# Performance work log

Measured on AMD Instinct MI355X. Metric: run time of the kernel, lower is better.

Reference implementation:

```python
import jax, jax.numpy as jnp
import numpy as np

B, P, C, H, W = 2, 4, 3, 256, 256
BGH, BGW = 2764, 3856
NOISE_MU, NOISE_SIGMA, NOISE_POISSON, BG_RATIO = 5.0, 1.0, 2.0, 0.1


def setup_inputs() -> dict:
    key = jax.random.key(0)
    k_x, k_bg = jax.random.split(key, 2)
    x = jax.random.uniform(k_x, (B, P, C, H, W), dtype=jnp.float32)
    t = jnp.array([0.05, 0.1, 0.15, 0.2], dtype=jnp.float32)          # Time_init (len p)
    ratio = jnp.ones((P,), dtype=jnp.float32)
    life = jnp.array([100.0, 200.0, 300.0], dtype=jnp.float32)         # flo_life (len c)
    intensity_ratio = jnp.array([1.0, 0.8, 0.6], dtype=jnp.float32)    # flo_intensity_ratio
    bg_file = jax.random.uniform(k_bg, (P, BGH, BGW), dtype=jnp.float32)
    return {"x": x, "t": t, "ratio": ratio, "life": life,
            "intensity_ratio": intensity_ratio, "bg_file": bg_file}


def reference(x, t, ratio, life, intensity_ratio, bg_file):
    b, p, c, h, w = x.shape
    key = jax.random.key(42)
    k_life, k_sig, k_norm, k_p1, k_p2, k_bg1, k_bg2, k_bgn, k_idx = jax.random.split(key, 9)

    # Time = relu((t*ratio)*1000), per-p scalar broadcast over (b,c,h,w)
    Time = jnp.maximum((t * ratio) * 1000.0, 0.0)                      # (p,)

    # tao_i: 9-point linspace around each lifetime, concatenated -> (T,) with T = 9*c
    tao = (life[:, None] + jnp.linspace(-40.0, 40.0, 9)).reshape(-1)   # (9c,)

    Life = life[None, None, :, None, None]                             # (1,1,c,1,1)
    Life_rand = Life + (jax.random.uniform(k_life, (b, p, c, h, w)) - 0.5) * 2.0 * 6.0
    sigma = 6.0
    sigma_rand = sigma + (jax.random.uniform(k_sig, (b, p, c, h, w)) - 0.5) * 2.0 * sigma * 0.05

    tao6 = tao[:, None, None, None, None, None]                        # (T,1,1,1,1,1)
    # Gaussian weights over the tao axis (matches torch's 3.14 constant)
    w_i = jnp.exp(-(tao6 - Life_rand) ** 2 / (2.0 * sigma_rand ** 2)) / (
        jnp.sqrt(jnp.float32(2.0 * 3.14)) * sigma_rand)                # (T,b,p,c,h,w)
    w_i = w_i / w_i.sum(axis=0)

    # tao_gt: sum over c, mean over p, permute -> (b,T,h,w), detached
    tao_gt = jax.lax.stop_gradient(jnp.transpose(w_i.sum(axis=3).mean(axis=2), (1, 0, 2, 3)))

    # decay_metrics = sum_T w_i * exp(-Time/tao); exp term only depends on (T,p)
    et = jnp.exp(-Time[None, :] / tao[:, None])                        # (T,p)
    decay = jnp.einsum('tp,tbpchw->bpchw', et, w_i)                    # (b,p,c,h,w)

    x2 = (x * decay * intensity_ratio[None, None, :, None, None]).sum(axis=2)  # (b,p,h,w)

    # noise(): Normal + Poisson(x/max) + Poisson(const) + x (samples detached in torch)
    xm = x2 / (x2.max() + 0.0001)
    n_int = xm * NOISE_MU + NOISE_SIGMA * jax.random.normal(k_norm, x2.shape)
    p_int = jax.random.poisson(k_p1, jnp.maximum(xm, 0.0)).astype(x2.dtype)
    pois = jax.random.poisson(k_p2, jnp.full(x2.shape, NOISE_POISSON)).astype(x2.dtype)
    x3 = n_int + p_int + pois + x2

    # bg(): scaled background file + noise, random 256x256 row offset
    bg1 = jax.random.uniform(k_bg1, (b, p, 1, 1)) * 0.5 + 0.5
    bg2 = jax.random.uniform(k_bg2, (b, p, 1, 1)) * 0.5 + 0.5
    bgn = jax.random.normal(k_bgn, (b, p, BGH, BGW))
    GRR = (bg_file[None] * bg1 + bgn * bg2) * BG_RATIO                 # (b,p,BGH,BGW)
    idx = jax.random.randint(k_idx, (), 0, 9)
    patch = jax.lax.dynamic_slice(GRR, (0, 0, idx, 0), (b, p, 256, 256))
    x4 = jnp.clip(x3 + patch, 0.0, 255.0) / 255.0

    return (x4, tao_gt, t * ratio, ratio)
```

## Files before the change

kernel.cpp:

```cpp
#include <hip/hip_runtime.h>
#include <cstdint>
#include <cstddef>

#define BB 2
#define PP 4
#define CC 3
#define HWSZ 65536
#define BGH 2764
#define BGW 3856
#define NTAO 27
#define X4_SIZE (BB*PP*HWSZ)
#define TAO_OFF X4_SIZE
#define TAO_SIZE (BB*NTAO*HWSZ)
#define OUT2_OFF (TAO_OFF + TAO_SIZE)
#define NPK 24
#define NBLK_A 2048

__host__ __device__ inline uint32_t rotl32(uint32_t x, int r) {
#ifdef __HIP_DEVICE_COMPILE__
  return __builtin_amdgcn_alignbit(x, x, 32 - r);
#else
  return (x << r) | (x >> (32 - r));
#endif
}

__host__ __device__ inline void tf2x32(uint32_t k0, uint32_t k1,
                                       uint32_t x0, uint32_t x1,
                                       uint32_t& o0, uint32_t& o1) {
  uint32_t ks2 = k0 ^ k1 ^ 0x1BD11BDAu;
  x0 += k0; x1 += k1;
#define TF_RND(r) { x0 += x1; x1 = rotl32(x1, r); x1 ^= x0; }
  TF_RND(13) TF_RND(15) TF_RND(26) TF_RND(6)
  x0 += k1;  x1 += ks2 + 1u;
  TF_RND(17) TF_RND(29) TF_RND(16) TF_RND(24)
  x0 += ks2; x1 += k0 + 2u;
  TF_RND(13) TF_RND(15) TF_RND(26) TF_RND(6)
  x0 += k0;  x1 += k1 + 3u;
  TF_RND(17) TF_RND(29) TF_RND(16) TF_RND(24)
  x0 += k1;  x1 += ks2 + 4u;
  TF_RND(13) TF_RND(15) TF_RND(26) TF_RND(6)
  x0 += ks2; x1 += k0 + 5u;
#undef TF_RND
  o0 = x0; o1 = x1;
}

__host__ __device__ inline uint32_t bits32(uint32_t k0, uint32_t k1, uint32_t e) {
  uint32_t o0, o1;
  tf2x32(k0, k1, 0u, e, o0, o1);
  return o0 ^ o1;
}

static void jax_split(uint32_t k0, uint32_t k1, int n, uint32_t (*keys)[2]) {
  for (int i = 0; i < n; ++i)
    tf2x32(k0, k1, 0u, (uint32_t)i, keys[i][0], keys[i][1]);
}

__host__ __device__ inline float u01(uint32_t bits) {
  uint32_t fb = (bits >> 9) | 0x3F800000u;
  return __builtin_bit_cast(float, fb) - 1.0f;
}

__device__ inline float erfinv_f(float x) {
  float w = -__logf(fmaf(-x, x, 1.0f));
  float p;
  if (w < 5.0f) {
    w = w - 2.5f;
    p = 2.81022636e-08f;
    p = fmaf(p, w, 3.43273939e-07f);
    p = fmaf(p, w, -3.5233877e-06f);
    p = fmaf(p, w, -4.39150654e-06f);
    p = fmaf(p, w, 0.00021858087f);
    p = fmaf(p, w, -0.00125372503f);
    p = fmaf(p, w, -0.00417768164f);
    p = fmaf(p, w, 0.246640727f);
    p = fmaf(p, w, 1.50140941f);
  } else {
    w = __builtin_amdgcn_sqrtf(w) - 3.0f;
    p = -0.000200214257f;
    p = fmaf(p, w, 0.000100950558f);
    p = fmaf(p, w, 0.00134934322f);
    p = fmaf(p, w, -0.00367342844f);
    p = fmaf(p, w, 0.00573950773f);
    p = fmaf(p, w, -0.0076224613f);
    p = fmaf(p, w, 0.00943887047f);
    p = fmaf(p, w, 1.00167406f);
    p = fmaf(p, w, 2.83297682f);
  }
  return p * x;
}

__device__ inline float normal_e(uint32_t k0, uint32_t k1, uint32_t e) {
  float f = u01(bits32(k0, k1, e));
  const float LO = -0.99999994f;
  float u = fmaxf(LO, fmaf(f, 2.0f, LO));
  return 1.41421356237f * erfinv_f(u);
}

struct PCParams {
  uint32_t kn0, kn1;
  uint32_t kb0, kb1;
  uint32_t s1[NPK * 2];
  uint32_t s2[NPK * 2];
  float bg1[8], bg2[8];
  int idx;
};

__device__ inline int pk_count2(const uint32_t* __restrict__ sk,
                                uint32_t e, float T) {
  float P = 1.0f;
  int cnt = 0;
#pragma clang loop unroll(disable)
  for (int i = 0; i < NPK; i += 2) {
    if (!__any(P > T)) break;
    float u0 = u01(bits32(sk[2*i],     sk[2*i+1],     e));
    float u1 = u01(bits32(sk[2*i+2],   sk[2*i+3],     e));
    float P0 = P * u0;
    float P1 = P0 * u1;
    cnt += (P0 > T) ? 1 : 0;
    cnt += (P1 > T) ? 1 : 0;
    P = P1;
  }
  return cnt;
}

__device__ inline float decay_pc(uint32_t kl0, uint32_t kl1, uint32_t ks0,
                                 uint32_t ks1, uint32_t e,
                                 const float (*et)[4], int p, float* tg9) {
  float ul = u01(bits32(kl0, kl1, e));
  float us = u01(bits32(ks0, ks1, e));
  float d0 = -40.0f - (ul - 0.5f) * 12.0f;
  float sr = fmaf(us - 0.5f, 0.6f, 6.0f);
  float inv = __builtin_amdgcn_rcpf(2.0f * sr * sr);
  float q[9];
  float A  = __expf(-20.0f * inv * d0);
  float Bm = __expf(-100.0f * inv);
  float B2 = Bm * Bm;
  q[0] = __expf(-(d0 * d0) * inv);
  float m = A * Bm;
  float s = q[0];
#pragma unroll
  for (int j = 1; j < 9; ++j) {
    q[j] = q[j - 1] * m;
    m *= B2;
    s += q[j];
  }
  float rs = __builtin_amdgcn_rcpf(s);
  float dec = 0.0f;
#pragma unroll
  for (int j = 0; j < 9; ++j) {
    float wn = q[j] * rs;
    tg9[j] += wn;
    dec = fmaf(et[j][p], wn, dec);
  }
  return dec;
}

__global__ __launch_bounds__(256) void kA(
    const float* __restrict__ x, const float* __restrict__ t,
    const float* __restrict__ ratio, const float* __restrict__ life,
    const float* __restrict__ inten, float* __restrict__ out,
    float* __restrict__ bmax,
    uint32_t kl0, uint32_t kl1, uint32_t ks0, uint32_t ks1) {
  __shared__ float et_s[NTAO][4];
  __shared__ float inten_s[3];
  __shared__ float tg_lds[4][9][64];
  __shared__ float bmax_s[4];
  const int tid = threadIdx.x;
  if (tid < NTAO * 4) {
    int j = tid >> 2, p = tid & 3;
    float tao = life[j / 9] + (-40.0f + 10.0f * (float)(j % 9));
    float Tp = fmaxf(t[p] * ratio[p] * 1000.0f, 0.0f);
    et_s[j][p] = expf((-Tp) / tao);
  }
  if (tid < 3) inten_s[tid] = inten[tid];
  __syncthreads();

  const int blk = blockIdx.x;
  const int b = blk >> 10;
  const int hwg = blk & 1023;
  const int p = tid >> 6;
  const int lane = tid & 63;
  const int hw = hwg * 64 + lane;

  float acc = 0.0f;

  for (int c = 0; c < 3; ++c) {
    float tg9[9];
#pragma unroll
    for (int j = 0; j < 9; ++j) tg9[j] = 0.0f;

    const uint32_t e = (uint32_t)((((b * 4 + p) * 3 + c) << 16) + hw);
    float dec = decay_pc(kl0, kl1, ks0, ks1, e,
                         (const float(*)[4])&et_s[c * 9], p, tg9);
    acc = fmaf(x[e] * dec, inten_s[c], acc);

#pragma unroll
    for (int j = 0; j < 9; ++j) tg_lds[p][j][lane] = tg9[j];
    __syncthreads();
    for (int jj = p; jj < 9; jj += 4) {
      float s = ((tg_lds[0][jj][lane] + tg_lds[1][jj][lane]) +
                 (tg_lds[2][jj][lane] + tg_lds[3][jj][lane]));
      out[TAO_OFF + ((b * NTAO + c * 9 + jj) << 16) + hw] = s * 0.25f;
    }
    __syncthreads();
  }

  out[((b * 4 + p) << 16) + hw] = acc;

  float m = acc;
#pragma unroll
  for (int off = 32; off; off >>= 1) m = fmaxf(m, __shfl_xor(m, off));
  if (lane == 0) bmax_s[p] = m;
  __syncthreads();
  if (tid == 0)
    bmax[blk] = fmaxf(fmaxf(bmax_s[0], bmax_s[1]),
                      fmaxf(bmax_s[2], bmax_s[3]));
}

__global__ __launch_bounds__(256) void kC(
    const float* __restrict__ bgf, const float* __restrict__ t,
    const float* __restrict__ ratio, float* __restrict__ out,
    const float* __restrict__ bmax, PCParams pc) {
  __shared__ float red_s[4];
  __shared__ float mx_s;
  const int tid = threadIdx.x;

  float m = 0.0f;
#pragma unroll
  for (int k = 0; k < 8; ++k) m = fmaxf(m, bmax[tid + 256 * k]);
#pragma unroll
  for (int off = 32; off; off >>= 1) m = fmaxf(m, __shfl_xor(m, off));
  if ((tid & 63) == 0) red_s[tid >> 6] = m;
  __syncthreads();
  if (tid == 0)
    mx_s = fmaxf(fmaxf(red_s[0], red_s[1]), fmaxf(red_s[2], red_s[3]));
  __syncthreads();
  const float mx = mx_s;

  if (blockIdx.x == 0 && tid < 8)
    out[OUT2_OFF + tid] = (tid < 4) ? t[tid] * ratio[tid] : ratio[tid - 4];

  const int e = blockIdx.x * 256 + tid;
  const int bp = e >> 16;
  const int rcc = e & 0xFFFF;
  const int r = rcc >> 8;
  const int cc = rcc & 255;

  const int row = pc.idx + r;
  const int p = bp & 3;
  const float bg = bgf[(p * BGH + row) * BGW + cc];
  const float x2 = out[e];

  const uint32_t ebg = (uint32_t)((bp * BGH + row) * BGW + cc);
  float nb = normal_e(pc.kb0, pc.kb1, ebg);
  float n  = normal_e(pc.kn0, pc.kn1, (uint32_t)e);
  float patch = (bg * pc.bg1[bp] + nb * pc.bg2[bp]) * 0.1f;

  const float xm = x2 * __builtin_amdgcn_rcpf(mx + 0.0001f);
  float n_int = fmaf(xm, 5.0f, n);

  const float lam1 = fmaxf(xm, 0.0f);
  const bool z1 = !(lam1 > 0.0f);
  float pi = 0.0f;
  if (!z1) {
    float T1 = __expf(-lam1);
    pi = (float)pk_count2(pc.s1, (uint32_t)e, T1);
  }
  const float T2 = 0.13533528f;
  float po = (float)pk_count2(pc.s2, (uint32_t)e, T2);

  float x3 = ((n_int + pi) + po) + x2;
  float v = x3 + patch;
  v = fminf(fmaxf(v, 0.0f), 255.0f);
  out[e] = v * (1.0f / 255.0f);
}

extern "C" void kernel_launch(void* const* d_in, const int* in_sizes, int n_in,
                              void* d_out, int out_size, void* d_ws, size_t ws_size,
                              hipStream_t stream) {
  const float* x     = (const float*)d_in[0];
  const float* t     = (const float*)d_in[1];
  const float* ratio = (const float*)d_in[2];
  const float* life  = (const float*)d_in[3];
  const float* inten = (const float*)d_in[4];
  const float* bgf   = (const float*)d_in[5];
  float* out = (float*)d_out;
  float* bmax = (float*)d_ws;

  uint32_t sk[9][2];
  jax_split(0u, 42u, 9, sk);

  PCParams pc;
  pc.kn0 = sk[2][0]; pc.kn1 = sk[2][1];
  pc.kb0 = sk[7][0]; pc.kb1 = sk[7][1];

  {
    uint32_t r0 = sk[3][0], r1 = sk[3][1];
    for (int i = 0; i < NPK; ++i) {
      uint32_t two[2][2];
      jax_split(r0, r1, 2, two);
      pc.s1[2*i] = two[1][0]; pc.s1[2*i+1] = two[1][1];
      r0 = two[0][0]; r1 = two[0][1];
    }
    r0 = sk[4][0]; r1 = sk[4][1];
    for (int i = 0; i < NPK; ++i) {
      uint32_t two[2][2];
      jax_split(r0, r1, 2, two);
      pc.s2[2*i] = two[1][0]; pc.s2[2*i+1] = two[1][1];
      r0 = two[0][0]; r1 = two[0][1];
    }
  }

  for (uint32_t i = 0; i < 8; ++i) {
    pc.bg1[i] = u01(bits32(sk[5][0], sk[5][1], i)) * 0.5f + 0.5f;
    pc.bg2[i] = u01(bits32(sk[6][0], sk[6][1], i)) * 0.5f + 0.5f;
  }

  {
    uint32_t hi = bits32(sk[8][0], sk[8][1], 0u);
    uint32_t lo = bits32(sk[8][0], sk[8][1], 1u);
    const uint32_t span = 9u;
    uint32_t mult = (65536u % span);
    mult = (mult * mult) % span;
    uint32_t off = ((hi % span) * mult + (lo % span)) % span;
    pc.idx = (int)off;
  }

  kA<<<NBLK_A, 256, 0, stream>>>(x, t, ratio, life, inten, out, bmax,
                                 sk[0][0], sk[0][1], sk[1][0], sk[1][1]);
  kC<<<X4_SIZE / 256, 256, 0, stream>>>(bgf, t, ratio, out, bmax, pc);
}
```

Measured before the change: 36.43 us.

## Fuse decay and noise kernels into one cooperative kernel with grid sync

Merges the two-kernel pipeline into a single cooperative launch of 1024 blocks. Each block processes two 64-pixel groups and keeps the x2 values in registers across a grid-wide sync, so the intermediate is never written to and re-read from global memory. The separate second launch also goes away. In exchange there is a grid barrier, a launch bound of 4 blocks per CU, and fewer blocks overall, which may reduce latency hiding in the RNG-heavy second phase.

```diff
diff --git a/kernel.cpp b/kernel.cpp
--- a/kernel.cpp
+++ b/kernel.cpp
@@ -1,6 +1,9 @@
 #include <hip/hip_runtime.h>
+#include <hip/hip_cooperative_groups.h>
 #include <cstdint>
 #include <cstddef>
+
+namespace cg = cooperative_groups;
 
 #define BB 2
 #define PP 4
@@ -14,7 +17,7 @@
 #define TAO_SIZE (BB*NTAO*HWSZ)
 #define OUT2_OFF (TAO_OFF + TAO_SIZE)
 #define NPK 24
-#define NBLK_A 2048
+#define NBLK_F 1024
 
 __host__ __device__ inline uint32_t rotl32(uint32_t x, int r) {
 #ifdef __HIP_DEVICE_COMPILE__
@@ -112,8 +115,8 @@
 #pragma clang loop unroll(disable)
   for (int i = 0; i < NPK; i += 2) {
     if (!__any(P > T)) break;
-    float u0 = u01(bits32(sk[2*i],     sk[2*i+1],     e));
-    float u1 = u01(bits32(sk[2*i+2],   sk[2*i+3],     e));
+    float u0 = u01(bits32(sk[2*i],   sk[2*i+1], e));
+    float u1 = u01(bits32(sk[2*i+2], sk[2*i+3], e));
     float P0 = P * u0;
     float P1 = P0 * u1;
     cnt += (P0 > T) ? 1 : 0;
@@ -155,16 +158,18 @@
   return dec;
 }
 
-__global__ __launch_bounds__(256) void kA(
+__global__ __launch_bounds__(256, 4) void kFused(
     const float* __restrict__ x, const float* __restrict__ t,
     const float* __restrict__ ratio, const float* __restrict__ life,
-    const float* __restrict__ inten, float* __restrict__ out,
-    float* __restrict__ bmax,
-    uint32_t kl0, uint32_t kl1, uint32_t ks0, uint32_t ks1) {
+    const float* __restrict__ inten, const float* __restrict__ bgf,
+    float* __restrict__ out, float* __restrict__ bmax,
+    uint32_t kl0, uint32_t kl1, uint32_t ks0, uint32_t ks1, PCParams pc) {
   __shared__ float et_s[NTAO][4];
   __shared__ float inten_s[3];
   __shared__ float tg_lds[4][9][64];
   __shared__ float bmax_s[4];
+  __shared__ float red_s[4];
+  __shared__ float mx_s;
   const int tid = threadIdx.x;
   if (tid < NTAO * 4) {
     int j = tid >> 2, p = tid & 3;
@@ -175,104 +180,108 @@
   if (tid < 3) inten_s[tid] = inten[tid];
   __syncthreads();
 
-  const int blk = blockIdx.x;
-  const int b = blk >> 10;
-  const int hwg = blk & 1023;
   const int p = tid >> 6;
   const int lane = tid & 63;
-  const int hw = hwg * 64 + lane;
-
-  float acc = 0.0f;
-
-  for (int c = 0; c < 3; ++c) {
-    float tg9[9];
-#pragma unroll
-    for (int j = 0; j < 9; ++j) tg9[j] = 0.0f;
-
-    const uint32_t e = (uint32_t)((((b * 4 + p) * 3 + c) << 16) + hw);
-    float dec = decay_pc(kl0, kl1, ks0, ks1, e,
-                         (const float(*)[4])&et_s[c * 9], p, tg9);
-    acc = fmaf(x[e] * dec, inten_s[c], acc);
-
-#pragma unroll
-    for (int j = 0; j < 9; ++j) tg_lds[p][j][lane] = tg9[j];
+
+  float accv0 = 0.0f, accv1 = 0.0f;
+#pragma unroll
+  for (int g2 = 0; g2 < 2; ++g2) {
+    const int vblk = blockIdx.x * 2 + g2;
+    const int b = vblk >> 10;
+    const int hwg = vblk & 1023;
+    const int hw = hwg * 64 + lane;
+
+    float acc = 0.0f;
+    for (int c = 0; c < 3; ++c) {
+      float tg9[9];
+#pragma unroll
+      for (int j = 0; j < 9; ++j) tg9[j] = 0.0f;
+
+      const uint32_t e = (uint32_t)((((b * 4 + p) * 3 + c) << 16) + hw);
+      float dec = decay_pc(kl0, kl1, ks0, ks1, e,
+                           (const float(*)[4])&et_s[c * 9], p, tg9);
+      acc = fmaf(x[e] * dec, inten_s[c], acc);
+
+#pragma unroll
+      for (int j = 0; j < 9; ++j) tg_lds[p][j][lane] = tg9[j];
+      __syncthreads();
+      for (int jj = p; jj < 9; jj += 4) {
+        float s = ((tg_lds[0][jj][lane] + tg_lds[1][jj][lane]) +
+                   (tg_lds[2][jj][lane] + tg_lds[3][jj][lane]));
+        out[TAO_OFF + ((b * NTAO + c * 9 + jj) << 16) + hw] = s * 0.25f;
+      }
+      __syncthreads();
+    }
+    if (g2 == 0) accv0 = acc; else accv1 = acc;
+  }
+
+  {
+    float m = fmaxf(accv0, accv1);
+#pragma unroll
+    for (int off = 32; off; off >>= 1) m = fmaxf(m, __shfl_xor(m, off));
+    if (lane == 0) bmax_s[p] = m;
     __syncthreads();
-    for (int jj = p; jj < 9; jj += 4) {
-      float s = ((tg_lds[0][jj][lane] + tg_lds[1][jj][lane]) +
-                 (tg_lds[2][jj][lane] + tg_lds[3][jj][lane]));
-      out[TAO_OFF + ((b * NTAO + c * 9 + jj) << 16) + hw] = s * 0.25f;
-    }
+    if (tid == 0)
+      bmax[blockIdx.x] = fmaxf(fmaxf(bmax_s[0], bmax_s[1]),
+                               fmaxf(bmax_s[2], bmax_s[3]));
+  }
+
+  cg::this_grid().sync();
+
+  {
+    float m = fmaxf(fmaxf(bmax[tid], bmax[tid + 256]),
+                    fmaxf(bmax[tid + 512], bmax[tid + 768]));
+#pragma unroll
+    for (int off = 32; off; off >>= 1) m = fmaxf(m, __shfl_xor(m, off));
+    if ((tid & 63) == 0) red_s[tid >> 6] = m;
     __syncthreads();
-  }
-
-  out[((b * 4 + p) << 16) + hw] = acc;
-
-  float m = acc;
-#pragma unroll
-  for (int off = 32; off; off >>= 1) m = fmaxf(m, __shfl_xor(m, off));
-  if (lane == 0) bmax_s[p] = m;
-  __syncthreads();
-  if (tid == 0)
-    bmax[blk] = fmaxf(fmaxf(bmax_s[0], bmax_s[1]),
-                      fmaxf(bmax_s[2], bmax_s[3]));
-}
-
-__global__ __launch_bounds__(256) void kC(
-    const float* __restrict__ bgf, const float* __restrict__ t,
-    const float* __restrict__ ratio, float* __restrict__ out,
-    const float* __restrict__ bmax, PCParams pc) {
-  __shared__ float red_s[4];
-  __shared__ float mx_s;
-  const int tid = threadIdx.x;
-
-  float m = 0.0f;
-#pragma unroll
-  for (int k = 0; k < 8; ++k) m = fmaxf(m, bmax[tid + 256 * k]);
-#pragma unroll
-  for (int off = 32; off; off >>= 1) m = fmaxf(m, __shfl_xor(m, off));
-  if ((tid & 63) == 0) red_s[tid >> 6] = m;
-  __syncthreads();
-  if (tid == 0)
-    mx_s = fmaxf(fmaxf(red_s[0], red_s[1]), fmaxf(red_s[2], red_s[3]));
-  __syncthreads();
+    if (tid == 0)
+      mx_s = fmaxf(fmaxf(red_s[0], red_s[1]), fmaxf(red_s[2], red_s[3]));
+    __syncthreads();
+  }
   const float mx = mx_s;
 
   if (blockIdx.x == 0 && tid < 8)
     out[OUT2_OFF + tid] = (tid < 4) ? t[tid] * ratio[tid] : ratio[tid - 4];
 
-  const int e = blockIdx.x * 256 + tid;
-  const int bp = e >> 16;
-  const int rcc = e & 0xFFFF;
-  const int r = rcc >> 8;
-  const int cc = rcc & 255;
-
-  const int row = pc.idx + r;
-  const int p = bp & 3;
-  const float bg = bgf[(p * BGH + row) * BGW + cc];
-  const float x2 = out[e];
-
-  const uint32_t ebg = (uint32_t)((bp * BGH + row) * BGW + cc);
-  float nb = normal_e(pc.kb0, pc.kb1, ebg);
-  float n  = normal_e(pc.kn0, pc.kn1, (uint32_t)e);
-  float patch = (bg * pc.bg1[bp] + nb * pc.bg2[bp]) * 0.1f;
-
-  const float xm = x2 * __builtin_amdgcn_rcpf(mx + 0.0001f);
-  float n_int = fmaf(xm, 5.0f, n);
-
-  const float lam1 = fmaxf(xm, 0.0f);
-  const bool z1 = !(lam1 > 0.0f);
-  float pi = 0.0f;
-  if (!z1) {
-    float T1 = __expf(-lam1);
-    pi = (float)pk_count2(pc.s1, (uint32_t)e, T1);
-  }
-  const float T2 = 0.13533528f;
-  float po = (float)pk_count2(pc.s2, (uint32_t)e, T2);
-
-  float x3 = ((n_int + pi) + po) + x2;
-  float v = x3 + patch;
-  v = fminf(fmaxf(v, 0.0f), 255.0f);
-  out[e] = v * (1.0f / 255.0f);
+#pragma unroll
+  for (int g2 = 0; g2 < 2; ++g2) {
+    const int vblk = blockIdx.x * 2 + g2;
+    const int b = vblk >> 10;
+    const int hwg = vblk & 1023;
+    const int hw = hwg * 64 + lane;
+    const int bp = b * 4 + p;
+    const int e = (bp << 16) + hw;
+    const float x2 = (g2 == 0) ? accv0 : accv1;
+
+    const int r = hw >> 8;
+    const int cc = hw & 255;
+    const int row = pc.idx + r;
+    const float bg = bgf[(p * BGH + row) * BGW + cc];
+
+    const uint32_t ebg = (uint32_t)((bp * BGH + row) * BGW + cc);
+    float nb = normal_e(pc.kb0, pc.kb1, ebg);
+    float n  = normal_e(pc.kn0, pc.kn1, (uint32_t)e);
+    float patch = (bg * pc.bg1[bp] + nb * pc.bg2[bp]) * 0.1f;
+
+    const float xm = x2 * __builtin_amdgcn_rcpf(mx + 0.0001f);
+    float n_int = fmaf(xm, 5.0f, n);
+
+    const float lam1 = fmaxf(xm, 0.0f);
+    const bool z1 = !(lam1 > 0.0f);
+    float pi = 0.0f;
+    if (!z1) {
+      float T1 = __expf(-lam1);
+      pi = (float)pk_count2(pc.s1, (uint32_t)e, T1);
+    }
+    const float T2 = 0.13533528f;
+    float po = (float)pk_count2(pc.s2, (uint32_t)e, T2);
+
+    float x3 = ((n_int + pi) + po) + x2;
+    float v = x3 + patch;
+    v = fminf(fmaxf(v, 0.0f), 255.0f);
+    out[e] = v * (1.0f / 255.0f);
+  }
 }
 
 extern "C" void kernel_launch(void* const* d_in, const int* in_sizes, int n_in,
@@ -326,7 +335,12 @@
     pc.idx = (int)off;
   }
 
-  kA<<<NBLK_A, 256, 0, stream>>>(x, t, ratio, life, inten, out, bmax,
-                                 sk[0][0], sk[0][1], sk[1][0], sk[1][1]);
-  kC<<<X4_SIZE / 256, 256, 0, stream>>>(bgf, t, ratio, out, bmax, pc);
-}
+  uint32_t kl0 = sk[0][0], kl1 = sk[0][1], ks0 = sk[1][0], ks1 = sk[1][1];
+  void* args[] = {
+    (void*)&x, (void*)&t, (void*)&ratio, (void*)&life, (void*)&inten,
+    (void*)&bgf, (void*)&out, (void*)&bmax,
+    (void*)&kl0, (void*)&kl1, (void*)&ks0, (void*)&ks1, (void*)&pc
+  };
+  hipLaunchCooperativeKernel((const void*)kFused, dim3(NBLK_F), dim3(256),
+                             args, 0, stream);
+}
```

After: 144.3 us. 296% more time.

## Process two elements per thread and flatten Poisson loops into one task queue

Applied to the files above, without the earlier changes.

kC now handles two output elements per thread with half the blocks. The four Poisson sampling loops (two lambdas times two elements) are merged into one state-machine loop that moves through the tasks, so lanes that finish one count early start the next instead of idling in a divergent wave. Poisson keys are staged in LDS so lookups can use a per-lane dynamic index. The cost is added per-iteration bookkeeping and LDS reads, and all four sequential PRNG chains now run in one loop, which may lengthen the critical path.

```diff
diff --git a/kernel.cpp b/kernel.cpp
--- a/kernel.cpp
+++ b/kernel.cpp
@@ -15,6 +15,7 @@
 #define OUT2_OFF (TAO_OFF + TAO_SIZE)
 #define NPK 24
 #define NBLK_A 2048
+#define NBLK_C 1024
 
 __host__ __device__ inline uint32_t rotl32(uint32_t x, int r) {
 #ifdef __HIP_DEVICE_COMPILE__
@@ -105,24 +106,6 @@
   int idx;
 };
 
-__device__ inline int pk_count2(const uint32_t* __restrict__ sk,
-                                uint32_t e, float T) {
-  float P = 1.0f;
-  int cnt = 0;
-#pragma clang loop unroll(disable)
-  for (int i = 0; i < NPK; i += 2) {
-    if (!__any(P > T)) break;
-    float u0 = u01(bits32(sk[2*i],     sk[2*i+1],     e));
-    float u1 = u01(bits32(sk[2*i+2],   sk[2*i+3],     e));
-    float P0 = P * u0;
-    float P1 = P0 * u1;
-    cnt += (P0 > T) ? 1 : 0;
-    cnt += (P1 > T) ? 1 : 0;
-    P = P1;
-  }
-  return cnt;
-}
-
 __device__ inline float decay_pc(uint32_t kl0, uint32_t kl1, uint32_t ks0,
                                  uint32_t ks1, uint32_t e,
                                  const float (*et)[4], int p, float* tg9) {
@@ -223,7 +206,13 @@
     const float* __restrict__ bmax, PCParams pc) {
   __shared__ float red_s[4];
   __shared__ float mx_s;
+  __shared__ uint32_t keys_lds[2 * NPK * 2];
   const int tid = threadIdx.x;
+
+  if (tid < NPK * 2) {
+    keys_lds[tid] = pc.s1[tid];
+    keys_lds[NPK * 2 + tid] = pc.s2[tid];
+  }
 
   float m = 0.0f;
 #pragma unroll
@@ -236,43 +225,89 @@
     mx_s = fmaxf(fmaxf(red_s[0], red_s[1]), fmaxf(red_s[2], red_s[3]));
   __syncthreads();
   const float mx = mx_s;
+  const float rmx = __builtin_amdgcn_rcpf(mx + 0.0001f);
 
   if (blockIdx.x == 0 && tid < 8)
     out[OUT2_OFF + tid] = (tid < 4) ? t[tid] * ratio[tid] : ratio[tid - 4];
 
-  const int e = blockIdx.x * 256 + tid;
-  const int bp = e >> 16;
-  const int rcc = e & 0xFFFF;
-  const int r = rcc >> 8;
-  const int cc = rcc & 255;
-
-  const int row = pc.idx + r;
-  const int p = bp & 3;
-  const float bg = bgf[(p * BGH + row) * BGW + cc];
-  const float x2 = out[e];
-
-  const uint32_t ebg = (uint32_t)((bp * BGH + row) * BGW + cc);
-  float nb = normal_e(pc.kb0, pc.kb1, ebg);
-  float n  = normal_e(pc.kn0, pc.kn1, (uint32_t)e);
-  float patch = (bg * pc.bg1[bp] + nb * pc.bg2[bp]) * 0.1f;
-
-  const float xm = x2 * __builtin_amdgcn_rcpf(mx + 0.0001f);
-  float n_int = fmaf(xm, 5.0f, n);
-
-  const float lam1 = fmaxf(xm, 0.0f);
-  const bool z1 = !(lam1 > 0.0f);
-  float pi = 0.0f;
-  if (!z1) {
-    float T1 = __expf(-lam1);
-    pi = (float)pk_count2(pc.s1, (uint32_t)e, T1);
-  }
+  const int gid = blockIdx.x * 256 + tid;
+  const int e0 = gid;
+  const int e1 = gid + X4_SIZE / 2;
+
+  const int bp0 = e0 >> 16, bp1 = e1 >> 16;
+  const int hw0 = e0 & 0xFFFF, hw1 = e1 & 0xFFFF;
+  const int r0 = hw0 >> 8, cc0 = hw0 & 255;
+  const int r1 = hw1 >> 8, cc1 = hw1 & 255;
+  const int row0 = pc.idx + r0, row1 = pc.idx + r1;
+  const int pp0 = bp0 & 3, pp1 = bp1 & 3;
+
+  const float x2_0 = out[e0];
+  const float x2_1 = out[e1];
+  const float bg0 = bgf[(pp0 * BGH + row0) * BGW + cc0];
+  const float bg1v = bgf[(pp1 * BGH + row1) * BGW + cc1];
+
+  const uint32_t ebg0 = (uint32_t)((bp0 * BGH + row0) * BGW + cc0);
+  const uint32_t ebg1 = (uint32_t)((bp1 * BGH + row1) * BGW + cc1);
+  float nb0 = normal_e(pc.kb0, pc.kb1, ebg0);
+  float nb1 = normal_e(pc.kb0, pc.kb1, ebg1);
+  float n0  = normal_e(pc.kn0, pc.kn1, (uint32_t)e0);
+  float n1  = normal_e(pc.kn0, pc.kn1, (uint32_t)e1);
+  float patch0 = (bg0  * pc.bg1[bp0] + nb0 * pc.bg2[bp0]) * 0.1f;
+  float patch1 = (bg1v * pc.bg1[bp1] + nb1 * pc.bg2[bp1]) * 0.1f;
+
+  const float xm0 = x2_0 * rmx;
+  const float xm1 = x2_1 * rmx;
   const float T2 = 0.13533528f;
-  float po = (float)pk_count2(pc.s2, (uint32_t)e, T2);
-
-  float x3 = ((n_int + pi) + po) + x2;
-  float v = x3 + patch;
-  v = fminf(fmaxf(v, 0.0f), 255.0f);
-  out[e] = v * (1.0f / 255.0f);
+  const float T1_0 = __expf(-fmaxf(xm0, 0.0f));
+  const float T1_1 = __expf(-fmaxf(xm1, 0.0f));
+
+  int tsk = 0, i = 0;
+  float P = 1.0f;
+  float T = T1_0;
+  uint32_t cnts = 0;
+#pragma clang loop unroll(disable)
+  for (int guard = 0; guard < 4 * NPK + 4; ++guard) {
+    bool active = (tsk < 4);
+    if (!__any(active)) break;
+    int kaddr = ((tsk & 1) * NPK + i) * 2;
+    uint32_t key0 = keys_lds[kaddr];
+    uint32_t key1 = keys_lds[kaddr + 1];
+    uint32_t ee = (tsk < 2) ? (uint32_t)e0 : (uint32_t)e1;
+    float u = u01(bits32(key0, key1, ee));
+    float Pn = P * u;
+    bool succ = active && (Pn > T);
+    if (succ) cnts += (1u << (tsk * 8));
+    bool advance = active && (!succ || i == NPK - 1);
+    if (active) P = Pn;
+    if (advance) {
+      tsk += 1;
+      i = 0;
+      P = 1.0f;
+      T = (tsk & 1) ? T2 : T1_1;
+    } else if (active) {
+      i += 1;
+    }
+  }
+
+  const float pi0 = (float)(cnts & 255u);
+  const float po0 = (float)((cnts >> 8) & 255u);
+  const float pi1 = (float)((cnts >> 16) & 255u);
+  const float po1 = (float)(cnts >> 24);
+
+  {
+    float n_int = fmaf(xm0, 5.0f, n0);
+    float x3 = ((n_int + pi0) + po0) + x2_0;
+    float v = x3 + patch0;
+    v = fminf(fmaxf(v, 0.0f), 255.0f);
+    out[e0] = v * (1.0f / 255.0f);
+  }
+  {
+    float n_int = fmaf(xm1, 5.0f, n1);
+    float x3 = ((n_int + pi1) + po1) + x2_1;
+    float v = x3 + patch1;
+    v = fminf(fmaxf(v, 0.0f), 255.0f);
+    out[e1] = v * (1.0f / 255.0f);
+  }
 }
 
 extern "C" void kernel_launch(void* const* d_in, const int* in_sizes, int n_in,
@@ -328,5 +363,5 @@
 
   kA<<<NBLK_A, 256, 0, stream>>>(x, t, ratio, life, inten, out, bmax,
                                  sk[0][0], sk[0][1], sk[1][0], sk[1][1]);
-  kC<<<X4_SIZE / 256, 256, 0, stream>>>(bgf, t, ratio, out, bmax, pc);
-}
+  kC<<<NBLK_C, 256, 0, stream>>>(bgf, t, ratio, out, bmax, pc);
+}
```

After: 34.72 us. 1.05x faster.
